# Performance work log

Hardware: AMD Instinct MI355X
Metric: run time of the kernel (lower is better)

Reference implementation:

```python
import jax, jax.numpy as jnp
import numpy as np
from jax import lax

SCALES = [0.5, 0.25, 0.125, 0.0625]
D_MODEL = 256
IN_CH = 1


def setup_inputs() -> dict:
    key = jax.random.key(0)
    ks = jax.random.split(key, 16)
    x = jax.random.normal(ks[0], (2, D_MODEL, 256, 256), dtype=jnp.float32)
    m = jax.random.uniform(ks[1], (2, IN_CH, 256, 256), dtype=jnp.float32)
    s = 0.05
    Wq = jax.random.normal(ks[2], (D_MODEL, D_MODEL, 1, 1), jnp.float32) * s
    bq = jax.random.normal(ks[3], (D_MODEL,), jnp.float32) * s
    Wk = jax.random.normal(ks[4], (D_MODEL, D_MODEL, 1, 1), jnp.float32) * s
    bk = jax.random.normal(ks[5], (D_MODEL,), jnp.float32) * s
    Wv = jax.random.normal(ks[6], (D_MODEL, D_MODEL, 1, 1), jnp.float32) * s
    bv = jax.random.normal(ks[7], (D_MODEL,), jnp.float32) * s
    Wmq = jax.random.normal(ks[8], (D_MODEL, IN_CH, 1, 1), jnp.float32) * s
    bmq = jax.random.normal(ks[9], (D_MODEL,), jnp.float32) * s
    Wmk = jax.random.normal(ks[10], (D_MODEL, IN_CH, 1, 1), jnp.float32) * s
    bmk = jax.random.normal(ks[11], (D_MODEL,), jnp.float32) * s
    Wo = jax.random.normal(ks[12], (D_MODEL, D_MODEL, 3, 3), jnp.float32) * s
    bo = jax.random.normal(ks[13], (D_MODEL,), jnp.float32) * s
    return {"x": x, "m": m, "Wq": Wq, "bq": bq, "Wk": Wk, "bk": bk,
            "Wv": Wv, "bv": bv, "Wmq": Wmq, "bmq": bmq, "Wmk": Wmk, "bmk": bmk,
            "Wo": Wo, "bo": bo, "b": 1, "c": 256}


def _conv1x1(z, W, bias):
    # W: (O, I, 1, 1)
    return jnp.einsum('bihw,oi->bohw', z, W[:, :, 0, 0]) + bias[None, :, None, None]


def _forward(x, m, Wq, bq, Wk, bk, Wv, bv, Wmq, bmq, Wmk, bmk, Wo, bo, b, c):
    bt, _, h, w = x.shape  # h, w are multiples of 64 -> pad is zero
    t = bt // b
    n_scales = len(SCALES)
    d_k = c // n_scales

    q = _conv1x1(x, Wq, bq)
    k = _conv1x1(x, Wk, bk)
    v = _conv1x1(x, Wv, bv)
    mq = _conv1x1(m, Wmq, bmq)
    mk = _conv1x1(m, Wmk, bmk)

    outs = []
    for i, scale in enumerate(SCALES):
        height, width = int(h * scale), int(w * scale)
        out_h, out_w = h // height, w // width
        sl = slice(i * d_k, (i + 1) * d_k)

        def patch(z):
            # (b, t, d_k, out_h, height, out_w, width) -> (b, t*out_h*out_w, d_k*height*width)
            z = z[:, sl].reshape(b, t, d_k, out_h, height, out_w, width)
            z = z.transpose(0, 1, 3, 5, 2, 4, 6)
            return z.reshape(b, t * out_h * out_w, d_k * height * width)

        Q, K, V = patch(q), patch(k), patch(v)
        MQ, MK = patch(mq), patch(mk)
        inv_sqrt_d = 1.0 / jnp.sqrt(jnp.asarray(Q.shape[-1], jnp.float32))
        scores = jnp.einsum('bnd,bmd->bnm', Q, K) * inv_sqrt_d
        mask_scores = jnp.einsum('bnd,bmd->bnm', MQ, MK) * inv_sqrt_d
        p_attn = jax.nn.softmax(scores * mask_scores, axis=-1)
        y = jnp.einsum('bnm,bmd->bnd', p_attn, V)
        # back to (bt, d_k, h, w)
        y = y.reshape(b, t, out_h, out_w, d_k, height, width)
        y = y.transpose(0, 1, 4, 2, 5, 3, 6).reshape(bt, d_k, h, w)
        outs.append(y)

    out = jnp.concatenate(outs, axis=1)
    z = lax.conv_general_dilated(out, Wo, window_strides=(1, 1),
                                 padding=((1, 1), (1, 1)),
                                 dimension_numbers=('NCHW', 'OIHW', 'NCHW'))
    z = z + bo[None, :, None, None]
    return jnp.where(z > 0, z, 0.2 * z)  # LeakyReLU(0.2)


def reference(x, m, Wq, bq, Wk, bk, Wv, bv, Wmq, bmq, Wmk, bmk, Wo, bo, b, c):
    return _forward(x, m, Wq, bq, Wk, bk, Wv, bv, Wmq, bmq, Wmk, bmk, Wo, bo, b, c)
```

## Files before the change

kernel.cpp:

```cpp
#include <hip/hip_runtime.h>
#include <stdint.h>


typedef __attribute__((ext_vector_type(8))) short short8;
typedef __attribute__((ext_vector_type(4))) float floatx4;
typedef __attribute__((ext_vector_type(4))) unsigned int uintx4;

#define DEV static __device__ __forceinline__

DEV unsigned short f2bf(float f) {
  unsigned u = __builtin_bit_cast(unsigned, f);
  unsigned r = u + 0x7FFFu + ((u >> 16) & 1u);
  return (unsigned short)(r >> 16);
}

DEV void patch_row(int n, int sc, int lw, int& pt, int& sp0) {
  pt = n >> (2 + 2 * sc);
  int rem = n & ((4 << (2 * sc)) - 1);
  int oh = rem >> (1 + sc), ow = rem & ((2 << sc) - 1);
  sp0 = (oh << (lw + 8)) + (ow << lw);
}

__global__ void k_prep_w(const float* __restrict__ Wq, const float* __restrict__ Wk,
                         const float* __restrict__ Wv, const float* __restrict__ bq,
                         const float* __restrict__ bk, const float* __restrict__ bv,
                         const float* __restrict__ Wmq, const float* __restrict__ bmq,
                         const float* __restrict__ Wmk, const float* __restrict__ bmk,
                         unsigned short* __restrict__ wqkv, float* __restrict__ bias,
                         float* __restrict__ msc) {
  int b = blockIdx.x;
  int t = threadIdx.x;
  if (b < 768) {
    const float* src = b < 256 ? (Wq + b * 256) : (b < 512 ? (Wk + (b - 256) * 256)
                                                           : (Wv + (b - 512) * 256));
    wqkv[b * 256 + t] = f2bf(src[t]);
    if (t == 0) bias[b] = b < 256 ? bq[b] : (b < 512 ? bk[b - 256] : bv[b - 512]);
  } else {
    int sc = t >> 6, lane = t & 63;
    int ch = sc * 64 + lane;
    float a0 = Wmq[ch] * Wmk[ch];
    float a1 = Wmq[ch] * bmk[ch];
    float a2 = bmq[ch] * Wmk[ch];
    float a3 = bmq[ch] * bmk[ch];
    for (int off = 32; off; off >>= 1) {
      a0 += __shfl_xor(a0, off); a1 += __shfl_xor(a1, off);
      a2 += __shfl_xor(a2, off); a3 += __shfl_xor(a3, off);
    }
    if (lane == 0) {
      msc[sc * 4 + 0] = a0; msc[sc * 4 + 1] = a1;
      msc[sc * 4 + 2] = a2; msc[sc * 4 + 3] = a3;
    }
  }
}

__global__ void k_prep_wo(const float* __restrict__ Wo, unsigned short* __restrict__ wobf,
                          float* __restrict__ scoresG, unsigned int* __restrict__ pbuf) {
  int blk = blockIdx.x;
  if (blk < 2304) {
    int didx = blk >> 8, o = blk & 255, c = threadIdx.x;
    wobf[didx * 65536 + o * 256 + c] = f2bf(Wo[o * 2304 + c * 9 + didx]);
  } else {
    int i = (blk - 2304) * 256 + threadIdx.x;
    if (i < 559232) scoresG[i] = 0.f;
    if (i < 140032) pbuf[i] = 0u;
  }
}

__global__ __launch_bounds__(256) void k_xt(const float* __restrict__ x,
                                            unsigned short* __restrict__ xt) {
  __shared__ __align__(16) unsigned short tile[64][72];
  int p0 = blockIdx.x * 64, c0 = blockIdx.y * 64, t = blockIdx.z;
  int tid = threadIdx.x;
  {
    int cc = tid >> 2, pq = (tid & 3) * 16;
    const float* src = x + ((t * 256 + c0 + cc) * 65536 + p0 + pq);
    __align__(16) unsigned short tmp[16];
#pragma unroll
    for (int e = 0; e < 16; e += 4) {
      floatx4 v = *(const floatx4*)(src + e);
      tmp[e + 0] = f2bf(v[0]); tmp[e + 1] = f2bf(v[1]);
      tmp[e + 2] = f2bf(v[2]); tmp[e + 3] = f2bf(v[3]);
    }
    *(uintx4*)&tile[cc][pq] = *(const uintx4*)&tmp[0];
    *(uintx4*)&tile[cc][pq + 8] = *(const uintx4*)&tmp[8];
  }
  __syncthreads();
  {
    int pp = tid >> 2, cg = (tid & 3) * 16;
    __align__(16) unsigned short outv[16];
#pragma unroll
    for (int e = 0; e < 16; ++e) outv[e] = tile[cg + e][pp];
    unsigned short* dst = xt + ((t * 65536 + p0 + pp) * 256 + c0 + cg);
    *(uintx4*)dst = *(const uintx4*)&outv[0];
    *(uintx4*)(dst + 8) = *(const uintx4*)&outv[8];
  }
}

__global__ __launch_bounds__(256) void k_yt(const unsigned short* __restrict__ ynat,
                                            unsigned short* __restrict__ yt) {
  __shared__ __align__(16) unsigned short tile[64][72];
  int p0 = blockIdx.x * 64, c0 = blockIdx.y * 64, t = blockIdx.z;
  int tid = threadIdx.x;
  {
    int cc = tid >> 2, pq = (tid & 3) * 16;
    const unsigned short* src = ynat + ((t * 256 + c0 + cc) * 65536 + p0 + pq);
    *(uintx4*)&tile[cc][pq] = *(const uintx4*)src;
    *(uintx4*)&tile[cc][pq + 8] = *(const uintx4*)(src + 8);
  }
  __syncthreads();
  {
    int pp = tid >> 2, cg = (tid & 3) * 16;
    __align__(16) unsigned short outv[16];
#pragma unroll
    for (int e = 0; e < 16; ++e) outv[e] = tile[cg + e][pp];
    unsigned short* dst = yt + ((t * 65536 + p0 + pp) * 256 + c0 + cg);
    *(uintx4*)dst = *(const uintx4*)&outv[0];
    *(uintx4*)(dst + 8) = *(const uintx4*)&outv[8];
  }
}

__global__ __launch_bounds__(256, 2) void k_qkv(const unsigned short* __restrict__ xt,
                                                const unsigned short* __restrict__ wqkv,
                                                const float* __restrict__ bias,
                                                unsigned short* __restrict__ qkv) {
  __shared__ __align__(16) unsigned short As[128][64];
  __shared__ __align__(16) unsigned short Bs[256][64];
  int flat = blockIdx.x;
  int lg = (flat & 7) * 384 + (flat >> 3);
  int n_t = lg / 6, m_t = lg - n_t * 6;
  int n0 = n_t << 8, m0 = m_t << 7;
  int tid = threadIdx.x;
  int w = tid >> 6, l = tid & 63;
  int wr = w >> 1, wc = w & 1;
  int l15 = l & 15, lhi = l >> 4;
  int sr = tid >> 1, sbase = (tid & 1) * 4, r7 = sr & 7;
  int b7 = tid & 7;
  const unsigned short* gA = wqkv + (m0 + sr) * 256 + sbase * 8;
  const unsigned short* gB = xt + (n0 + tid) * 256;
  floatx4 zf = {0.f, 0.f, 0.f, 0.f};
  floatx4 acc[4][8];
#pragma unroll
  for (int i = 0; i < 4; ++i)
#pragma unroll
    for (int j = 0; j < 8; ++j) acc[i][j] = zf;
  uintx4 ra[4], rb[8];
#define QLOAD(K0) { const uintx4* pa = (const uintx4*)(gA + (K0)); \
                    ra[0] = pa[0]; ra[1] = pa[1]; ra[2] = pa[2]; ra[3] = pa[3]; \
                    const uintx4* pb = (const uintx4*)(gB + (K0)); \
                    rb[0] = pb[0]; rb[1] = pb[1]; rb[2] = pb[2]; rb[3] = pb[3]; \
                    rb[4] = pb[4]; rb[5] = pb[5]; rb[6] = pb[6]; rb[7] = pb[7]; }
  QLOAD(0);
#pragma unroll
  for (int ch = 0; ch < 4; ++ch) {
    __syncthreads();
#pragma unroll
    for (int j = 0; j < 4; ++j)
      *(uintx4*)&As[sr][((sbase + j) ^ r7) * 8] = ra[j];
#pragma unroll
    for (int j = 0; j < 8; ++j)
      *(uintx4*)&Bs[tid][(j ^ b7) * 8] = rb[j];
    __syncthreads();
    if (ch < 3) QLOAD((ch + 1) * 64);
#pragma unroll
    for (int kk = 0; kk < 2; ++kk) {
      short8 af[4];
#pragma unroll
      for (int f = 0; f < 4; ++f) {
        int arow = wr * 64 + f * 16 + l15;
        af[f] = *(const short8*)&As[arow][(((kk << 2) + lhi) ^ (arow & 7)) * 8];
      }
#pragma unroll
      for (int fn = 0; fn < 8; ++fn) {
        int brow = wc * 128 + fn * 16 + l15;
        short8 b = *(const short8*)&Bs[brow][(((kk << 2) + lhi) ^ (brow & 7)) * 8];
#pragma unroll
        for (int fm = 0; fm < 4; ++fm)
          acc[fm][fn] = __builtin_amdgcn_mfma_f32_16x16x32_bf16(af[fm], b, acc[fm][fn], 0, 0, 0);
      }
    }
  }
#undef QLOAD
#pragma unroll
  for (int fm = 0; fm < 4; ++fm) {
    int crow = m0 + wr * 64 + fm * 16 + lhi * 4;
#pragma unroll
    for (int rr = 0; rr < 4; ++rr) {
      float bv = bias[crow + rr];
#pragma unroll
      for (int fn = 0; fn < 8; ++fn) {
        int pcol = n0 + wc * 128 + fn * 16 + l15;
        int t = pcol >> 16, p = pcol & 65535;
        qkv[(t * 768 + crow + rr) * 65536 + p] = f2bf(acc[fm][fn][rr] + bv);
      }
    }
  }
}

__global__ __launch_bounds__(256) void k_gram2(const float* __restrict__ m,
                                               float* __restrict__ G) {
  __shared__ __align__(16) float Ns[32][68];
  __shared__ __align__(16) float Ms[32][68];
  int bid = blockIdx.x;
  int sc, tn, tm, z, nchunks, soff;
  if (bid < 32)      { sc = 0; tn = 0; tm = 0; z = bid;      nchunks = 8; soff = 0; }
  else if (bid < 40) { sc = 1; tn = 0; tm = 0; z = bid - 32; nchunks = 8; soff = 64; }
  else if (bid < 72) { int r = bid - 40; int tl = r >> 1; sc = 2; tn = tl >> 2; tm = tl & 3; z = r & 1; nchunks = 8; soff = 1088; }
  else               { int tl = bid - 72; sc = 3; tn = tl >> 4; tm = tl & 15; z = 0; nchunks = 4; soff = 17472; }
  int lw = 7 - sc, W = 1 << lw, N = 8 << (2 * sc);
  int kbase = z * nchunks * 64;
  int n0 = tn * 32, m0 = tm * 32;
  int tid = threadIdx.x;
  bool isA = tid < 128;
  int u = tid & 127;
  int srow = u >> 2, sslot0 = (u & 3) * 4;
  int grow = (isA ? n0 : m0) + srow;
  bool valid = grow < N;
  int pt = 0, sp0 = 0;
  if (valid) patch_row(grow, sc, lw, pt, sp0);
  int gbase = pt * 65536 + sp0;
  int trc = tid >> 4, tcc = tid & 15;
  float a00 = 0.f, a01 = 0.f, a10 = 0.f, a11 = 0.f;
  floatx4 zf = {0.f, 0.f, 0.f, 0.f};
  for (int c = 0; c < nchunks; ++c) {
    int k0 = kbase + c * 64;
    floatx4 v[4];
#pragma unroll
    for (int j = 0; j < 4; ++j) {
      v[j] = zf;
      if (valid) {
        int s = k0 + (sslot0 + j) * 4;
        int hh = s >> lw, ww = s & (W - 1);
        v[j] = *(const floatx4*)(m + gbase + (hh << 8) + ww);
      }
    }
    __syncthreads();
    float* dstrow = isA ? &Ns[srow][0] : &Ms[srow][0];
#pragma unroll
    for (int j = 0; j < 4; ++j) *(floatx4*)&dstrow[(sslot0 + j) * 4] = v[j];
    __syncthreads();
#pragma unroll 4
    for (int k = 0; k < 64; k += 4) {
      floatx4 na = *(const floatx4*)&Ns[2 * trc][k];
      floatx4 nb = *(const floatx4*)&Ns[2 * trc + 1][k];
      floatx4 ma = *(const floatx4*)&Ms[2 * tcc][k];
      floatx4 mb = *(const floatx4*)&Ms[2 * tcc + 1][k];
#pragma unroll
      for (int e = 0; e < 4; ++e) {
        a00 += na[e] * ma[e]; a01 += na[e] * mb[e];
        a10 += nb[e] * ma[e]; a11 += nb[e] * mb[e];
      }
    }
  }
  int rn = n0 + 2 * trc, rm = m0 + 2 * tcc;
  float res[2][2] = {{a00, a01}, {a10, a11}};
#pragma unroll
  for (int i = 0; i < 2; ++i)
#pragma unroll
    for (int j = 0; j < 2; ++j) {
      if (rn + i < N && rm + j < N) {
        float* dst = &G[soff + (rn + i) * N + rm + j];
        if (sc < 3) atomicAdd(dst, res[i][j]); else *dst = res[i][j];
      }
    }
}

__global__ void k_rsum(const float* __restrict__ m, float* __restrict__ rbuf) {
  int row = blockIdx.x, lane = threadIdx.x;
  int sc, n;
  if (row < 8)        { sc = 0; n = row; }
  else if (row < 40)  { sc = 1; n = row - 8; }
  else if (row < 168) { sc = 2; n = row - 40; }
  else                { sc = 3; n = row - 168; }
  int lw = 7 - sc, W = 1 << lw;
  int pt, sp0;
  patch_row(n, sc, lw, pt, sp0);
  int base = pt * 65536 + sp0;
  int S = 1 << (14 - 2 * sc);
  float acc = 0.f;
  for (int s = lane; s < S; s += 64) {
    int hh = s >> lw, ww = s & (W - 1);
    acc += m[base + (hh << 8) + ww];
  }
  for (int off = 32; off; off >>= 1) acc += __shfl_xor(acc, off);
  if (lane == 0) rbuf[row] = acc;
}

__global__ __launch_bounds__(256) void k_scores2(const unsigned short* __restrict__ qkv,
                                                 float* __restrict__ scores) {
  __shared__ __align__(16) unsigned short As[32][136];
  __shared__ __align__(16) unsigned short Bs[32][136];
  int bid = blockIdx.x;
  int sc, tn, tm, z, soff;
  if (bid < 256)      { sc = 0; tn = 0; tm = 0; z = bid;       soff = 0; }
  else                { sc = 1; tn = 0; tm = 0; z = bid - 256; soff = 64; }
  int lw = 7 - sc, W = 1 << lw, lS = 14 - 2 * sc, N = 8 << (2 * sc);
  int n0 = tn * 32, m0 = tm * 32;
  int kbase = z * 4096;
  int tid = threadIdx.x, w = tid >> 6, l = tid & 63;
  int wr = w >> 1, wc = w & 1, l15 = l & 15, lhi = l >> 4;
  floatx4 acc = {0.f, 0.f, 0.f, 0.f};
  bool isA = tid < 128;
  int u = tid & 127;
  int srow = u >> 2, sslot0 = (u & 3) * 4;
  int grow = (isA ? n0 : m0) + srow;
  int cb = (isA ? 0 : 256) + sc * 64;
  int pt = 0, sp0 = 0;
  bool valid = grow < N;
  if (valid) patch_row(grow, sc, lw, pt, sp0);
  int rowbase = (pt * 768 + cb) * 65536 + sp0;
  uintx4 zu = {0u, 0u, 0u, 0u};
  uintx4 r[4];
#define SLOAD(KS) { int kb2 = kbase + (KS) * 128; \
  _Pragma("unroll") for (int j = 0; j < 4; ++j) { \
    uintx4 v = zu; \
    if (valid) { int k = kb2 + (sslot0 + j) * 8; \
      int cl = k >> lS; int s = k & ((1 << lS) - 1); \
      int hh = s >> lw, ww = s & (W - 1); \
      v = *(const uintx4*)(qkv + rowbase + cl * 65536 + (hh << 8) + ww); } \
    r[j] = v; } }
  SLOAD(0);
  for (int ks = 0; ks < 32; ++ks) {
    __syncthreads();
    {
      unsigned short* dstrow = isA ? &As[srow][0] : &Bs[srow][0];
#pragma unroll
      for (int j = 0; j < 4; ++j) *(uintx4*)&dstrow[(sslot0 + j) * 8] = r[j];
    }
    __syncthreads();
    if (ks < 31) SLOAD(ks + 1);
#pragma unroll
    for (int kk = 0; kk < 4; ++kk) {
      short8 a = *(const short8*)&As[wr * 16 + l15][(kk * 4 + lhi) * 8];
      short8 b = *(const short8*)&Bs[wc * 16 + l15][(kk * 4 + lhi) * 8];
      acc = __builtin_amdgcn_mfma_f32_16x16x32_bf16(a, b, acc, 0, 0, 0);
    }
  }
#undef SLOAD
  int rrow = n0 + wr * 16 + lhi * 4;
  int ccol = m0 + wc * 16 + l15;
  if (ccol < N) {
#pragma unroll
    for (int rr = 0; rr < 4; ++rr)
      if (rrow + rr < N) atomicAdd(&scores[soff + (rrow + rr) * N + ccol], acc[rr]);
  }
}

__global__ __launch_bounds__(256) void k_scores_big(const unsigned short* __restrict__ qkv,
                                                    float* __restrict__ scores) {
  __shared__ __align__(16) unsigned short As[128][64];
  __shared__ __align__(16) unsigned short Bs[128][64];
  int flat = blockIdx.x;
  int lg = (flat & 7) * 20 + (flat >> 3);
  int sc, tn, tm, z, soff;
  if (lg < 32) { sc = 2; tn = 0; tm = 0; z = lg; soff = 1088; }
  else { int r = lg - 32; int tl = r >> 3; sc = 3; tn = tl >> 2; tm = tl & 3; z = r & 7; soff = 17472; }
  int N = 8 << (2 * sc);
  int lw = 7 - sc, W = 1 << lw, lS = 14 - 2 * sc;
  int n0 = tn * 128, m0 = tm * 128;
  int kbase = z * 2048;
  int tid = threadIdx.x;
  int w = tid >> 6, l = tid & 63;
  int wr = w >> 1, wc = w & 1;
  int l15 = l & 15, lhi = l >> 4;
  int sr = tid >> 1, sbase = (tid & 1) * 4, r7 = sr & 7;
  int ptA, spA, ptB, spB;
  patch_row(n0 + sr, sc, lw, ptA, spA);
  patch_row(m0 + sr, sc, lw, ptB, spB);
  int baseA = (ptA * 768 + sc * 64) * 65536 + spA;
  int baseB = (ptB * 768 + 256 + sc * 64) * 65536 + spB;
  floatx4 zf = {0.f, 0.f, 0.f, 0.f};
  floatx4 acc[4][4];
#pragma unroll
  for (int i = 0; i < 4; ++i)
#pragma unroll
    for (int j = 0; j < 4; ++j) acc[i][j] = zf;
  uintx4 ra[4], rb[4];
#define GLOAD(K0) { \
  _Pragma("unroll") for (int j = 0; j < 4; ++j) { \
    int k = kbase + (K0) + (sbase + j) * 8; \
    int cl = k >> lS; int s = k & ((1 << lS) - 1); \
    int hh = s >> lw, ww = s & (W - 1); \
    int off = cl * 65536 + (hh << 8) + ww; \
    ra[j] = *(const uintx4*)(qkv + baseA + off); \
    rb[j] = *(const uintx4*)(qkv + baseB + off); } }
  GLOAD(0);
  for (int st = 0; st < 32; ++st) {
    __syncthreads();
#pragma unroll
    for (int j = 0; j < 4; ++j) {
      *(uintx4*)&As[sr][((sbase + j) ^ r7) * 8] = ra[j];
      *(uintx4*)&Bs[sr][((sbase + j) ^ r7) * 8] = rb[j];
    }
    __syncthreads();
    if (st < 31) GLOAD((st + 1) * 64);
#pragma unroll
    for (int kk = 0; kk < 2; ++kk) {
      short8 af[4], bfr[4];
#pragma unroll
      for (int f = 0; f < 4; ++f) {
        int arow = wr * 64 + f * 16 + l15;
        af[f] = *(const short8*)&As[arow][(((kk << 2) + lhi) ^ (arow & 7)) * 8];
        int brow = wc * 64 + f * 16 + l15;
        bfr[f] = *(const short8*)&Bs[brow][(((kk << 2) + lhi) ^ (brow & 7)) * 8];
      }
#pragma unroll
      for (int fm = 0; fm < 4; ++fm)
#pragma unroll
        for (int fn = 0; fn < 4; ++fn)
          acc[fm][fn] = __builtin_amdgcn_mfma_f32_16x16x32_bf16(af[fm], bfr[fn], acc[fm][fn], 0, 0, 0);
    }
  }
#undef GLOAD
#pragma unroll
  for (int fm = 0; fm < 4; ++fm) {
    int nrow = n0 + wr * 64 + fm * 16 + lhi * 4;
#pragma unroll
    for (int rr = 0; rr < 4; ++rr) {
#pragma unroll
      for (int fn = 0; fn < 4; ++fn) {
        int mcol = m0 + wc * 64 + fn * 16 + l15;
        atomicAdd(&scores[soff + (nrow + rr) * N + mcol], acc[fm][fn][rr]);
      }
    }
  }
}

__global__ void k_softmax(const float* __restrict__ scores, const float* __restrict__ G,
                          const float* __restrict__ rbuf, const float* __restrict__ msc,
                          unsigned short* __restrict__ pbuf) {
  int row = blockIdx.x, lane = threadIdx.x;
  int sc, n, roff, soff, poff;
  if (row < 8)        { sc = 0; n = row;       roff = 0;   soff = 0;     poff = 0; }
  else if (row < 40)  { sc = 1; n = row - 8;   roff = 8;   soff = 64;    poff = 512; }
  else if (row < 168) { sc = 2; n = row - 40;  roff = 40;  soff = 1088;  poff = 1536; }
  else                { sc = 3; n = row - 168; roff = 168; soff = 17472; poff = 17920; }
  int N = 8 << (2 * sc);
  int Kpad = (sc < 2) ? 32 : N;
  float Sf = (float)(1 << (14 - 2 * sc));
  float invD = 1.0f / (float)(1 << (20 - 2 * sc));
  float alpha = msc[sc * 4 + 0], beta = msc[sc * 4 + 1];
  float gamma = msc[sc * 4 + 2], delta = msc[sc * 4 + 3];
  float rn = rbuf[roff + n];
  float vals[8];
  float mx = -1e30f;
#pragma unroll
  for (int j = 0; j < 8; ++j) {
    float v = -1e30f;
    int mcol = lane + j * 64;
    if (j * 64 < N && mcol < N) {
      float sq = scores[soff + n * N + mcol];
      float g = G[soff + n * N + mcol];
      float rm = rbuf[roff + mcol];
      v = sq * (alpha * g + beta * rn + gamma * rm + delta * Sf) * invD;
    }
    vals[j] = v;
    mx = fmaxf(mx, v);
  }
  for (int off = 32; off; off >>= 1) mx = fmaxf(mx, __shfl_xor(mx, off));
  float sum = 0.f;
#pragma unroll
  for (int j = 0; j < 8; ++j) {
    int mcol = lane + j * 64;
    float e = 0.f;
    if (j * 64 < N && mcol < N) e = __expf(vals[j] - mx);
    vals[j] = e;
    sum += e;
  }
  for (int off = 32; off; off >>= 1) sum += __shfl_xor(sum, off);
  float inv = 1.f / sum;
#pragma unroll
  for (int j = 0; j < 8; ++j) {
    int mcol = lane + j * 64;
    if (j * 64 < N && mcol < N) pbuf[poff + n * Kpad + mcol] = f2bf(vals[j] * inv);
  }
}

__global__ __launch_bounds__(256) void k_pv(const unsigned short* __restrict__ qkv,
                                            const unsigned short* __restrict__ pbuf,
                                            unsigned short* __restrict__ ynat) {
  int bid = blockIdx.x;
  int sc, bx, by;
  if (bid < 4096)      { sc = 0; bx = bid; by = 0; }
  else if (bid < 6144) { sc = 1; bx = bid - 4096; by = 0; }
  else if (bid < 8192) { int r = bid - 6144; sc = 2; bx = r >> 1; by = r & 1; }
  else                 { int r = bid - 8192; sc = 3; bx = r >> 3; by = r & 7; }
  int WR    = (sc == 0) ? 1 : (sc == 1) ? 2 : 4;
  int logWC = (sc == 0) ? 2 : (sc == 1) ? 1 : 0;
  int poff  = (sc == 0) ? 0 : (sc == 1) ? 512 : (sc == 2) ? 1536 : 17920;
  int lw = 7 - sc, W = 1 << lw;
  int lS = 14 - 2 * sc;
  int N = 8 << (2 * sc);
  int Kpad = (sc < 2) ? 32 : N;
  int WC = 1 << logWC;
  int d0 = bx * (WC * 64);
  int nb = by * (WR * 16);
  __shared__ __align__(16) unsigned short As[2][64][40];
  __shared__ __align__(16) unsigned short Bt[2][256][32];
  int tid = threadIdx.x;
  int w = tid >> 6, l = tid & 63;
  int wr = w >> logWC, wc = w & (WC - 1);
  int l15 = l & 15, lhi = l >> 4;
  floatx4 zf = {0.f, 0.f, 0.f, 0.f};
  floatx4 acc[4];
#pragma unroll
  for (int i = 0; i < 4; ++i) acc[i] = zf;
  int bmp = tid & 15;
  int dg = tid >> 4;
  bool act0 = (WC > 1) || (dg < 8);
  bool has1 = (WC == 4);
  bool doA = tid < WR * 64;
  int arow = tid >> 2, akg = (tid & 3) * 8;
  int ksteps = Kpad >> 5;
  uintx4 zu = {0u, 0u, 0u, 0u};
  int vcb = (512 + sc * 64) * 65536;
  uintx4 av = zu, lo0 = zu, hi0 = zu, lo1 = zu, hi1 = zu;
#define PLOADS(KS) { int k0 = (KS) * 32; \
    av = zu; lo0 = zu; hi0 = zu; lo1 = zu; hi1 = zu; \
    if (doA) av = *(const uintx4*)(pbuf + poff + (nb + arow) * Kpad + k0 + akg); \
    int gm0 = k0 + 2 * bmp, gm1 = gm0 + 1; \
    bool mv0 = gm0 < N, mv1 = gm1 < N; \
    int pt0 = 0, sp00 = 0, pt1 = 0, sp01 = 0; \
    if (mv0) patch_row(gm0, sc, lw, pt0, sp00); \
    if (mv1) patch_row(gm1, sc, lw, pt1, sp01); \
    { int d = d0 + dg * 8; int cl = d >> lS; int s = d & ((1 << lS) - 1); \
      int hh = s >> lw, ww = s & (W - 1); int sp = (hh << 8) + ww; \
      if (act0 && mv0) lo0 = *(const uintx4*)(qkv + pt0 * 768 * 65536 + vcb + cl * 65536 + sp00 + sp); \
      if (act0 && mv1) hi0 = *(const uintx4*)(qkv + pt1 * 768 * 65536 + vcb + cl * 65536 + sp01 + sp); } \
    if (has1) { int d = d0 + (dg + 16) * 8; int cl = d >> lS; int s = d & ((1 << lS) - 1); \
      int hh = s >> lw, ww = s & (W - 1); int sp = (hh << 8) + ww; \
      if (mv0) lo1 = *(const uintx4*)(qkv + pt0 * 768 * 65536 + vcb + cl * 65536 + sp00 + sp); \
      if (mv1) hi1 = *(const uintx4*)(qkv + pt1 * 768 * 65536 + vcb + cl * 65536 + sp01 + sp); } }
  PLOADS(0);
  for (int ks = 0; ks < ksteps; ++ks) {
    int b = ks & 1;
    if (doA) *(uintx4*)&As[b][arow][akg] = av;
    if (act0) {
      int du = dg * 8;
#pragma unroll
      for (int j = 0; j < 8; ++j) {
        int d = du + j;
        unsigned losh = (lo0[j >> 1] >> ((j & 1) * 16)) & 0xFFFFu;
        unsigned hish = (hi0[j >> 1] >> ((j & 1) * 16)) & 0xFFFFu;
        unsigned wv = losh | (hish << 16);
        int slot = (bmp >> 2) ^ ((d >> 1) & 3) ^ ((d >> 3) & 3);
        ((unsigned int*)&Bt[b][d][0])[slot * 4 + (bmp & 3)] = wv;
      }
    }
    if (has1) {
      int du = (dg + 16) * 8;
#pragma unroll
      for (int j = 0; j < 8; ++j) {
        int d = du + j;
        unsigned losh = (lo1[j >> 1] >> ((j & 1) * 16)) & 0xFFFFu;
        unsigned hish = (hi1[j >> 1] >> ((j & 1) * 16)) & 0xFFFFu;
        unsigned wv = losh | (hish << 16);
        int slot = (bmp >> 2) ^ ((d >> 1) & 3) ^ ((d >> 3) & 3);
        ((unsigned int*)&Bt[b][d][0])[slot * 4 + (bmp & 3)] = wv;
      }
    }
    __syncthreads();
    if (ks + 1 < ksteps) PLOADS(ks + 1);
    short8 a = *(const short8*)&As[b][wr * 16 + l15][lhi * 8];
#pragma unroll
    for (int fn = 0; fn < 4; ++fn) {
      int row = wc * 64 + fn * 16 + l15;
      int slot = lhi ^ ((row >> 1) & 3) ^ ((row >> 3) & 3);
      short8 bb = *(const short8*)&Bt[b][row][slot * 8];
      acc[fn] = __builtin_amdgcn_mfma_f32_16x16x32_bf16(a, bb, acc[fn], 0, 0, 0);
    }
  }
#undef PLOADS
  int nrow = nb + wr * 16 + lhi * 4;
#pragma unroll
  for (int rr = 0; rr < 4; ++rr) {
    int n = nrow + rr;
    if (n < N) {
      int pt, sp0;
      patch_row(n, sc, lw, pt, sp0);
#pragma unroll
      for (int fn = 0; fn < 4; ++fn) {
        int d = d0 + wc * 64 + fn * 16 + l15;
        int cl = d >> lS;
        int s = d & ((1 << lS) - 1);
        int hh = s >> lw, ww = s & (W - 1);
        int c = sc * 64 + cl;
        ynat[(pt * 256 + c) * 65536 + sp0 + (hh << 8) + ww] = f2bf(acc[fn][rr]);
      }
    }
  }
}

__global__ __launch_bounds__(256, 2) void k_conv(const unsigned short* __restrict__ yt,
                                                 const unsigned short* __restrict__ wo,
                                                 const float* __restrict__ bo,
                                                 float* __restrict__ out) {
  __shared__ __align__(16) unsigned short As[128][128];
  __shared__ __align__(16) unsigned short Bs[130][64];
  int flat = blockIdx.x;
  int lg = ((flat & 7) << 7) + (flat >> 3);
  int n_t = lg >> 1, m_t = lg & 1;
  int n0 = n_t << 8, m0 = m_t << 7;
  int tt = n0 >> 16, yy = (n0 >> 8) & 255;
  int tid = threadIdx.x;
  int w = tid >> 6, l = tid & 63;
  int wr = w >> 1, wc = w & 1;
  int l15 = l & 15, lhi = l >> 4;
  int a_d0 = tid >> 7, a_o0 = tid & 127;
  bool doA1 = tid < 128;
  bool doBh = tid >= 254;
  floatx4 zf = {0.f, 0.f, 0.f, 0.f};
  floatx4 acc[4][8];
#pragma unroll
  for (int i = 0; i < 4; ++i)
#pragma unroll
    for (int j = 0; j < 8; ++j) acc[i][j] = zf;
  uintx4 zu = {0u, 0u, 0u, 0u};
  uintx4 rb[4], ra0[4], ra1[4];
  const unsigned short* ybase = yt + (tt << 24);
#define CLOAD(ST) { \
    int dy = (ST) >> 3, cc = ((ST) & 7) << 5; \
    int yq = yy + dy - 1; \
    bool yv = (unsigned)yq < 256u; \
    { int xq = tid - 1; \
      if (yv && (unsigned)xq < 256u) { \
        const uintx4* p = (const uintx4*)(ybase + ((yq << 8) + xq) * 256 + cc); \
        rb[0] = p[0]; rb[1] = p[1]; rb[2] = p[2]; rb[3] = p[3]; \
      } else { rb[0] = zu; rb[1] = zu; rb[2] = zu; rb[3] = zu; } } \
    { const uintx4* p = (const uintx4*)(wo + (dy * 3 + a_d0) * 65536 + (m0 + a_o0) * 256 + cc); \
      ra0[0] = p[0]; ra0[1] = p[1]; ra0[2] = p[2]; ra0[3] = p[3]; } \
    if (doA1) { \
      const uintx4* p = (const uintx4*)(wo + (dy * 3 + 2) * 65536 + (m0 + tid) * 256 + cc); \
      ra1[0] = p[0]; ra1[1] = p[1]; ra1[2] = p[2]; ra1[3] = p[3]; \
    } else if (doBh) { \
      int xq = tid + 1; \
      if (yv && xq < 256) { \
        const uintx4* p = (const uintx4*)(ybase + ((yq << 8) + xq) * 256 + cc); \
        ra1[0] = p[0]; ra1[1] = p[1]; ra1[2] = p[2]; ra1[3] = p[3]; \
      } else { ra1[0] = zu; ra1[1] = zu; ra1[2] = zu; ra1[3] = zu; } } }
  CLOAD(0);
  for (int st = 0; st < 24; ++st) {
    __syncthreads();
    {
      int brow = tid >> 1, bhf = (tid & 1) * 4, br7 = brow & 7;
#pragma unroll
      for (int j = 0; j < 4; ++j)
        *(uintx4*)&Bs[brow][((bhf + j) ^ br7) * 8] = rb[j];
      int ao7 = a_o0 & 7;
#pragma unroll
      for (int j = 0; j < 4; ++j)
        *(uintx4*)&As[a_o0][((a_d0 * 4 + j) ^ ao7) * 8] = ra0[j];
      if (doA1) {
        int o7 = tid & 7;
#pragma unroll
        for (int j = 0; j < 4; ++j)
          *(uintx4*)&As[tid][((8 + j) ^ o7) * 8] = ra1[j];
      } else if (doBh) {
        int xh = tid + 2;
        int brow2 = xh >> 1, bhf2 = (xh & 1) * 4, br72 = brow2 & 7;
#pragma unroll
        for (int j = 0; j < 4; ++j)
          *(uintx4*)&Bs[brow2][((bhf2 + j) ^ br72) * 8] = ra1[j];
      }
    }
    __syncthreads();
    if (st < 23) CLOAD(st + 1);
#pragma unroll
    for (int dx = 0; dx < 3; ++dx) {
      short8 af[4];
#pragma unroll
      for (int f = 0; f < 4; ++f) {
        int ol = wr * 64 + f * 16 + l15;
        af[f] = *(const short8*)&As[ol][((dx * 4 + lhi) ^ (ol & 7)) * 8];
      }
#pragma unroll
      for (int fn = 0; fn < 8; ++fn) {
        int xh = wc * 128 + fn * 16 + l15 + dx;
        short8 b = *(const short8*)&Bs[xh >> 1][((((xh & 1) * 4 + lhi)) ^ ((xh >> 1) & 7)) * 8];
#pragma unroll
        for (int fm = 0; fm < 4; ++fm)
          acc[fm][fn] = __builtin_amdgcn_mfma_f32_16x16x32_bf16(af[fm], b, acc[fm][fn], 0, 0, 0);
      }
    }
  }
#undef CLOAD
#pragma unroll
  for (int fm = 0; fm < 4; ++fm) {
    int o = m0 + wr * 64 + fm * 16 + lhi * 4;
#pragma unroll
    for (int rr = 0; rr < 4; ++rr) {
      float bias = bo[o + rr];
#pragma unroll
      for (int fn = 0; fn < 8; ++fn) {
        int xcol = wc * 128 + fn * 16 + l15;
        float z = acc[fm][fn][rr] + bias;
        out[((tt * 256 + o + rr) << 16) + (yy << 8) + xcol] = z > 0.f ? z : 0.2f * z;
      }
    }
  }
}

extern "C" void kernel_launch(void* const* d_in, const int* in_sizes, int n_in,
                              void* d_out, int out_size, void* d_ws, size_t ws_size,
                              hipStream_t stream) {
  const float* x   = (const float*)d_in[0];
  const float* m   = (const float*)d_in[1];
  const float* Wq  = (const float*)d_in[2];
  const float* bq  = (const float*)d_in[3];
  const float* Wk  = (const float*)d_in[4];
  const float* bk  = (const float*)d_in[5];
  const float* Wv  = (const float*)d_in[6];
  const float* bv  = (const float*)d_in[7];
  const float* Wmq = (const float*)d_in[8];
  const float* bmq = (const float*)d_in[9];
  const float* Wmk = (const float*)d_in[10];
  const float* bmk = (const float*)d_in[11];
  const float* Wo  = (const float*)d_in[12];
  const float* bo  = (const float*)d_in[13];

  char* ws = (char*)d_ws;
  unsigned short* qkv   = (unsigned short*)(ws);
  unsigned short* xtb   = (unsigned short*)(ws + 201326592);
  unsigned short* wqkv  = (unsigned short*)(ws + 268435456);
  unsigned short* wobf  = (unsigned short*)(ws + 268828672);
  float* bias           = (float*)(ws + 270008320);
  float* msc            = (float*)(ws + 270011392);
  float* scores         = (float*)(ws + 270011456);
  float* G              = (float*)(ws + 271129920);
  float* rbuf           = (float*)(ws + 272248384);
  unsigned short* pbuf  = (unsigned short*)(ws + 272251104);
  float* out            = (float*)d_out;
  unsigned short* ynat  = (unsigned short*)d_out;

  k_prep_w<<<dim3(769), dim3(256), 0, stream>>>(Wq, Wk, Wv, bq, bk, bv, Wmq, bmq, Wmk, bmk,
                                                wqkv, bias, msc);
  k_prep_wo<<<dim3(4489), dim3(256), 0, stream>>>(Wo, wobf, scores, (unsigned int*)pbuf);
  k_xt<<<dim3(1024, 4, 2), dim3(256), 0, stream>>>(x, xtb);
  k_qkv<<<dim3(3072), dim3(256), 0, stream>>>(xtb, wqkv, bias, qkv);
  k_gram2<<<dim3(328), dim3(256), 0, stream>>>(m, G);
  k_rsum<<<dim3(680), dim3(64), 0, stream>>>(m, rbuf);
  k_scores2<<<dim3(320), dim3(256), 0, stream>>>(qkv, scores);
  k_scores_big<<<dim3(160), dim3(256), 0, stream>>>(qkv, scores);
  k_softmax<<<dim3(680), dim3(64), 0, stream>>>(scores, G, rbuf, msc, pbuf);
  k_pv<<<dim3(10240), dim3(256), 0, stream>>>(qkv, pbuf, ynat);
  k_yt<<<dim3(1024, 4, 2), dim3(256), 0, stream>>>(ynat, xtb);
  k_conv<<<dim3(1024), dim3(256), 0, stream>>>(xtb, wobf, bo, out);
}
```

Baseline: 577.3 us.

## Double-buffer conv input tile and read weight fragments straight from global

The conv kernel no longer stages weights in shared memory. Weights are repacked into an MFMA-fragment-friendly layout in the prep kernel and loaded per wave directly from global/L2 into registers, prefetched one dx step ahead. The input tile becomes double-buffered in LDS with register prefetch two stages ahead, which removes one barrier per stage and frees the 32KB A tile. The k_pv block index is also swizzled across XCDs. This trades repeated global weight reads and extra register pressure for fewer barriers and less LDS traffic.

```diff
diff --git a/kernel.cpp b/kernel.cpp
--- a/kernel.cpp
+++ b/kernel.cpp
@@ -58,7 +58,7 @@
   int blk = blockIdx.x;
   if (blk < 2304) {
     int didx = blk >> 8, o = blk & 255, c = threadIdx.x;
-    wobf[didx * 65536 + o * 256 + c] = f2bf(Wo[o * 2304 + c * 9 + didx]);
+    wobf[((didx * 8 + (c >> 5)) * 256 + o) * 32 + (c & 31)] = f2bf(Wo[o * 2304 + c * 9 + didx]);
   } else {
     int i = (blk - 2304) * 256 + threadIdx.x;
     if (i < 559232) scoresG[i] = 0.f;
@@ -478,7 +478,8 @@
 __global__ __launch_bounds__(256) void k_pv(const unsigned short* __restrict__ qkv,
                                             const unsigned short* __restrict__ pbuf,
                                             unsigned short* __restrict__ ynat) {
-  int bid = blockIdx.x;
+  int bid0 = blockIdx.x;
+  int bid = (bid0 & 7) * 1280 + (bid0 >> 3);
   int sc, bx, by;
   if (bid < 4096)      { sc = 0; bx = bid; by = 0; }
   else if (bid < 6144) { sc = 1; bx = bid - 4096; by = 0; }
@@ -591,11 +592,10 @@
 }
 
 __global__ __launch_bounds__(256, 2) void k_conv(const unsigned short* __restrict__ yt,
-                                                 const unsigned short* __restrict__ wo,
+                                                 const unsigned short* __restrict__ wo2,
                                                  const float* __restrict__ bo,
                                                  float* __restrict__ out) {
-  __shared__ __align__(16) unsigned short As[128][128];
-  __shared__ __align__(16) unsigned short Bs[130][64];
+  __shared__ __align__(16) unsigned short Bs[2][130][64];
   int flat = blockIdx.x;
   int lg = ((flat & 7) << 7) + (flat >> 3);
   int n_t = lg >> 1, m_t = lg & 1;
@@ -605,8 +605,6 @@
   int w = tid >> 6, l = tid & 63;
   int wr = w >> 1, wc = w & 1;
   int l15 = l & 15, lhi = l >> 4;
-  int a_d0 = tid >> 7, a_o0 = tid & 127;
-  bool doA1 = tid < 128;
   bool doBh = tid >= 254;
   floatx4 zf = {0.f, 0.f, 0.f, 0.f};
   floatx4 acc[4][8];
@@ -615,74 +613,66 @@
 #pragma unroll
     for (int j = 0; j < 8; ++j) acc[i][j] = zf;
   uintx4 zu = {0u, 0u, 0u, 0u};
-  uintx4 rb[4], ra0[4], ra1[4];
+  uintx4 rbA[4], rbB[4], rh[4];
   const unsigned short* ybase = yt + (tt << 24);
-#define CLOAD(ST) { \
-    int dy = (ST) >> 3, cc = ((ST) & 7) << 5; \
-    int yq = yy + dy - 1; \
-    bool yv = (unsigned)yq < 256u; \
-    { int xq = tid - 1; \
-      if (yv && (unsigned)xq < 256u) { \
-        const uintx4* p = (const uintx4*)(ybase + ((yq << 8) + xq) * 256 + cc); \
-        rb[0] = p[0]; rb[1] = p[1]; rb[2] = p[2]; rb[3] = p[3]; \
-      } else { rb[0] = zu; rb[1] = zu; rb[2] = zu; rb[3] = zu; } } \
-    { const uintx4* p = (const uintx4*)(wo + (dy * 3 + a_d0) * 65536 + (m0 + a_o0) * 256 + cc); \
-      ra0[0] = p[0]; ra0[1] = p[1]; ra0[2] = p[2]; ra0[3] = p[3]; } \
-    if (doA1) { \
-      const uintx4* p = (const uintx4*)(wo + (dy * 3 + 2) * 65536 + (m0 + tid) * 256 + cc); \
-      ra1[0] = p[0]; ra1[1] = p[1]; ra1[2] = p[2]; ra1[3] = p[3]; \
-    } else if (doBh) { \
-      int xq = tid + 1; \
-      if (yv && xq < 256) { \
-        const uintx4* p = (const uintx4*)(ybase + ((yq << 8) + xq) * 256 + cc); \
-        ra1[0] = p[0]; ra1[1] = p[1]; ra1[2] = p[2]; ra1[3] = p[3]; \
-      } else { ra1[0] = zu; ra1[1] = zu; ra1[2] = zu; ra1[3] = zu; } } }
-  CLOAD(0);
+  const unsigned short* wbase = wo2 + (m0 + wr * 64 + l15) * 32 + lhi * 8;
+#define CLB(ST, RB) { int dy_ = (ST) >> 3, cc_ = ((ST) & 7) << 5; \
+    int yq_ = yy + dy_ - 1; int xq_ = tid - 1; \
+    if (((unsigned)yq_ < 256u) && ((unsigned)xq_ < 256u)) { \
+      const uintx4* p_ = (const uintx4*)(ybase + ((yq_ << 8) + xq_) * 256 + cc_); \
+      RB[0] = p_[0]; RB[1] = p_[1]; RB[2] = p_[2]; RB[3] = p_[3]; \
+    } else { RB[0] = zu; RB[1] = zu; RB[2] = zu; RB[3] = zu; } }
+#define CLH(ST) { int dy_ = (ST) >> 3, cc_ = ((ST) & 7) << 5; \
+    int yq_ = yy + dy_ - 1; int xq_ = tid + 1; \
+    if (doBh && ((unsigned)yq_ < 256u) && (xq_ < 256)) { \
+      const uintx4* p_ = (const uintx4*)(ybase + ((yq_ << 8) + xq_) * 256 + cc_); \
+      rh[0] = p_[0]; rh[1] = p_[1]; rh[2] = p_[2]; rh[3] = p_[3]; \
+    } else { rh[0] = zu; rh[1] = zu; rh[2] = zu; rh[3] = zu; } }
+#define BWR(BUF, RB) { int brow_ = tid >> 1, bhf_ = (tid & 1) * 4, br7_ = brow_ & 7; \
+    _Pragma("unroll") for (int j = 0; j < 4; ++j) \
+      *(uintx4*)&Bs[BUF][brow_][((bhf_ + j) ^ br7_) * 8] = RB[j]; \
+    if (doBh) { int xh_ = tid + 2; int brow2_ = xh_ >> 1, bhf2_ = (xh_ & 1) * 4, br72_ = brow2_ & 7; \
+    _Pragma("unroll") for (int j = 0; j < 4; ++j) \
+      *(uintx4*)&Bs[BUF][brow2_][((bhf2_ + j) ^ br72_) * 8] = rh[j]; } }
+  CLB(0, rbA); CLH(0);
+  BWR(0, rbA);
+  CLB(1, rbB); CLH(1);
+  __syncthreads();
   for (int st = 0; st < 24; ++st) {
-    __syncthreads();
-    {
-      int brow = tid >> 1, bhf = (tid & 1) * 4, br7 = brow & 7;
-#pragma unroll
-      for (int j = 0; j < 4; ++j)
-        *(uintx4*)&Bs[brow][((bhf + j) ^ br7) * 8] = rb[j];
-      int ao7 = a_o0 & 7;
-#pragma unroll
-      for (int j = 0; j < 4; ++j)
-        *(uintx4*)&As[a_o0][((a_d0 * 4 + j) ^ ao7) * 8] = ra0[j];
-      if (doA1) {
-        int o7 = tid & 7;
-#pragma unroll
-        for (int j = 0; j < 4; ++j)
-          *(uintx4*)&As[tid][((8 + j) ^ o7) * 8] = ra1[j];
-      } else if (doBh) {
-        int xh = tid + 2;
-        int brow2 = xh >> 1, bhf2 = (xh & 1) * 4, br72 = brow2 & 7;
-#pragma unroll
-        for (int j = 0; j < 4; ++j)
-          *(uintx4*)&Bs[brow2][((bhf2 + j) ^ br72) * 8] = ra1[j];
-      }
-    }
-    __syncthreads();
-    if (st < 23) CLOAD(st + 1);
+    int cur = st & 1;
+    if (st < 23) { if (cur == 0) { BWR(1, rbB); } else { BWR(0, rbA); } }
+    if (st < 22) { if (cur == 0) { CLB(st + 2, rbA); } else { CLB(st + 2, rbB); } }
+    if (st < 22) { CLH(st + 2); }
+    int dy = st >> 3, ccs = st & 7;
+    const unsigned short* abase = wbase + ((dy * 3) * 8 + ccs) * 256 * 32;
+    short8 af[4], ag[4];
+#pragma unroll
+    for (int f = 0; f < 4; ++f) af[f] = *(const short8*)(abase + f * 512);
 #pragma unroll
     for (int dx = 0; dx < 3; ++dx) {
-      short8 af[4];
-#pragma unroll
-      for (int f = 0; f < 4; ++f) {
-        int ol = wr * 64 + f * 16 + l15;
-        af[f] = *(const short8*)&As[ol][((dx * 4 + lhi) ^ (ol & 7)) * 8];
+      if (dx < 2) {
+        const unsigned short* ab2 = abase + (dx + 1) * 65536;
+#pragma unroll
+        for (int f = 0; f < 4; ++f) ag[f] = *(const short8*)(ab2 + f * 512);
       }
 #pragma unroll
       for (int fn = 0; fn < 8; ++fn) {
         int xh = wc * 128 + fn * 16 + l15 + dx;
-        short8 b = *(const short8*)&Bs[xh >> 1][((((xh & 1) * 4 + lhi)) ^ ((xh >> 1) & 7)) * 8];
+        short8 b = *(const short8*)&Bs[cur][xh >> 1][((((xh & 1) * 4 + lhi)) ^ ((xh >> 1) & 7)) * 8];
 #pragma unroll
         for (int fm = 0; fm < 4; ++fm)
           acc[fm][fn] = __builtin_amdgcn_mfma_f32_16x16x32_bf16(af[fm], b, acc[fm][fn], 0, 0, 0);
       }
-    }
-  }
-#undef CLOAD
+      if (dx < 2) {
+#pragma unroll
+        for (int f = 0; f < 4; ++f) af[f] = ag[f];
+      }
+    }
+    __syncthreads();
+  }
+#undef CLB
+#undef CLH
+#undef BWR
 #pragma unroll
   for (int fm = 0; fm < 4; ++fm) {
     int o = m0 + wr * 64 + fm * 16 + lhi * 4;
```

New measurement: 706.5 us. 22.4% more time.
